# Performance work log

Measured on AMD Instinct MI355X. Metric: run time of the kernel, lower is better.

The kernel has to match this reference:

```python
import jax, jax.numpy as jnp
import numpy as np
import math

EMBED_DIM = 512
NHEAD = 8
HEAD_DIM = EMBED_DIM // NHEAD
B, L = 32, 512
EPS = 1e-5


def layer_norm(x, gamma, beta):
    mu = jnp.mean(x, axis=-1, keepdims=True)
    var = jnp.var(x, axis=-1, keepdims=True)
    return (x - mu) * jax.lax.rsqrt(var + EPS) * gamma + beta


def setup_inputs() -> dict:
    key = jax.random.key(0)
    ks = jax.random.split(key, 16)
    D = EMBED_DIM
    s = 1.0 / math.sqrt(D)
    return {
        "x": jax.random.normal(ks[0], (B, L, D), dtype=jnp.float32),
        "inter": jax.random.normal(ks[1], (B, L, L, 4), dtype=jnp.float32),
        "qkv_w": jax.random.normal(ks[2], (D, 3 * D), dtype=jnp.float32) * s,
        "qkv_b": jnp.zeros((3 * D,), dtype=jnp.float32),
        "out_w": jax.random.normal(ks[3], (D, D), dtype=jnp.float32) * s,
        "out_b": jnp.zeros((D,), dtype=jnp.float32),
        "norm1_g": jnp.ones((D,), dtype=jnp.float32),
        "norm1_b": jnp.zeros((D,), dtype=jnp.float32),
        "norm2_g": jnp.ones((D,), dtype=jnp.float32),
        "norm2_b": jnp.zeros((D,), dtype=jnp.float32),
        "inter_w": jax.random.normal(ks[4], (4, NHEAD), dtype=jnp.float32) * 0.5,
        "ffn_w1": jax.random.normal(ks[5], (D, 4 * D), dtype=jnp.float32) * s,
        "ffn_b1": jnp.zeros((4 * D,), dtype=jnp.float32),
        "ffn_w2": jax.random.normal(ks[6], (4 * D, D), dtype=jnp.float32) * (1.0 / math.sqrt(4 * D)),
        "ffn_b2": jnp.zeros((D,), dtype=jnp.float32),
    }


def reference(x, inter, qkv_w, qkv_b, out_w, out_b, norm1_g, norm1_b,
              norm2_g, norm2_b, inter_w, ffn_w1, ffn_b1, ffn_w2, ffn_b2):
    Bb, Ll, D = x.shape
    residual = x
    h = layer_norm(x, norm1_g, norm1_b)
    qkv = (h @ qkv_w + qkv_b).reshape(Bb, Ll, 3, NHEAD, HEAD_DIM)
    qkv = jnp.transpose(qkv, (2, 0, 3, 1, 4))  # (3, B, H, L, hd)
    q, k, v = qkv[0], qkv[1], qkv[2]
    scale = math.sqrt(HEAD_DIM)
    scores = jnp.einsum("bhqd,bhkd->bhqk", q, k) / scale
    # pairwise interaction bias: (B,L,L,4) @ (4,H) -> (B,H,L,L)
    bias = jnp.einsum("bqkf,fh->bhqk", inter, inter_w)
    attn = jax.nn.softmax(scores + bias, axis=-1)
    # dropout p=0 in eval mode
    out = jnp.einsum("bhqk,bhkd->bhqd", attn, v)
    out = jnp.transpose(out, (0, 2, 1, 3)).reshape(Bb, Ll, D)
    x = residual + out @ out_w + out_b
    h2 = layer_norm(x, norm2_g, norm2_b)
    ffn = jax.nn.gelu(h2 @ ffn_w1 + ffn_b1, approximate=False) @ ffn_w2 + ffn_b2
    return x + ffn
```

## Files before the change

kernel.cpp:

```cpp
#include <hip/hip_runtime.h>
#include <math.h>

#define BB 32
#define LL 512
#define DD 512
#define NH 8
#define HD 64

typedef __attribute__((ext_vector_type(8))) short bf16x8;
typedef __attribute__((ext_vector_type(4))) float f32x4;

__device__ __forceinline__ unsigned short f2bf(float x) {
    union { float f; unsigned u; } v; v.f = x;
    unsigned r = v.u + 0x7fffu + ((v.u >> 16) & 1u);
    return (unsigned short)(r >> 16);
}

__device__ __forceinline__ float warp_sum(float v) {
    #pragma unroll
    for (int o = 32; o > 0; o >>= 1) v += __shfl_down(v, o);
    return v;
}

__global__ void ln_kernel(const float* __restrict__ X, const float* __restrict__ g,
                          const float* __restrict__ b, unsigned short* __restrict__ Y) {
    __shared__ float red[8];
    const size_t base = (size_t)blockIdx.x * DD;
    const int t = threadIdx.x;
    float x0 = X[base + t], x1 = X[base + t + 256];
    float s = warp_sum(x0 + x1);
    float q = warp_sum(x0 * x0 + x1 * x1);
    if ((t & 63) == 0) { red[t >> 6] = s; red[4 + (t >> 6)] = q; }
    __syncthreads();
    float S = red[0] + red[1] + red[2] + red[3];
    float Q = red[4] + red[5] + red[6] + red[7];
    float mu  = S * (1.0f / 512.0f);
    float var = Q * (1.0f / 512.0f) - mu * mu;
    float r = rsqrtf(var + 1e-5f);
    Y[base + t]       = f2bf((x0 - mu) * r * g[t] + b[t]);
    Y[base + t + 256] = f2bf((x1 - mu) * r * g[t + 256] + b[t + 256]);
}

__global__ void transpose_bf16(const float* __restrict__ W, unsigned short* __restrict__ WT,
                               int K, int N) {
    __shared__ float t[32][33];
    const int n0 = blockIdx.x * 32, k0 = blockIdx.y * 32;
    const int tx = threadIdx.x & 31, ty = threadIdx.x >> 5;
    #pragma unroll
    for (int r = 0; r < 32; r += 8)
        t[ty + r][tx] = W[(size_t)(k0 + ty + r) * N + n0 + tx];
    __syncthreads();
    #pragma unroll
    for (int r = 0; r < 32; r += 8)
        WT[(size_t)(n0 + ty + r) * K + k0 + tx] = f2bf(t[tx][ty + r]);
}

template <int ACT, int RES, int OM>
__global__ __launch_bounds__(256)
void gemm_mfma(const unsigned short* __restrict__ A, const unsigned short* __restrict__ BT,
               const float* __restrict__ bias, const float* __restrict__ res,
               void* __restrict__ Cv, unsigned short* __restrict__ kfrag,
               unsigned short* __restrict__ vfrag, int M, int N, int K) {
    __shared__ unsigned short As0[128 * 64];
    __shared__ unsigned short Bs0[128 * 64];
    __shared__ unsigned short As1[128 * 64];
    __shared__ unsigned short Bs1[128 * 64];
    const int tid = threadIdx.x;
    const int wave = tid >> 6, lane = tid & 63;
    const int wm = (wave >> 1) * 64, wn = (wave & 1) * 64;

    const int nx = N >> 7;
    const int chunk = (int)gridDim.x >> 3;
    const int o = ((int)blockIdx.x & 7) * chunk + ((int)blockIdx.x >> 3);
    const int bn = (o % nx) * 128;
    const int bm = (o / nx) * 128;

    f32x4 acc[4][4] = {};

    auto stage = [&](unsigned short* AS, unsigned short* BS, int k0) {
        #pragma unroll
        for (int it = 0; it < 4; ++it) {
            const int s = it * 256 + tid;
            const int row = s >> 3, pch = s & 7;
            const int lch = pch ^ (row & 7);
            const unsigned short* ga = A + (size_t)(bm + row) * K + k0 + lch * 8;
            __builtin_amdgcn_global_load_lds(
                (const __attribute__((address_space(1))) void*)ga,
                (__attribute__((address_space(3))) void*)(AS + s * 8), 16, 0, 0);
            const unsigned short* gb = BT + (size_t)(bn + row) * K + k0 + lch * 8;
            __builtin_amdgcn_global_load_lds(
                (const __attribute__((address_space(1))) void*)gb,
                (__attribute__((address_space(3))) void*)(BS + s * 8), 16, 0, 0);
        }
    };

    auto compute = [&](const unsigned short* AS, const unsigned short* BS) {
        #pragma unroll
        for (int ks = 0; ks < 2; ++ks) {
            bf16x8 af[4], bfr[4];
            #pragma unroll
            for (int i = 0; i < 4; ++i) {
                const int row = wm + i * 16 + (lane & 15);
                const int pch = (ks * 4 + (lane >> 4)) ^ (row & 7);
                af[i] = *(const bf16x8*)(AS + row * 64 + pch * 8);
            }
            #pragma unroll
            for (int j = 0; j < 4; ++j) {
                const int row = wn + j * 16 + (lane & 15);
                const int pch = (ks * 4 + (lane >> 4)) ^ (row & 7);
                bfr[j] = *(const bf16x8*)(BS + row * 64 + pch * 8);
            }
            #pragma unroll
            for (int i = 0; i < 4; ++i)
                #pragma unroll
                for (int j = 0; j < 4; ++j)
                    acc[i][j] = __builtin_amdgcn_mfma_f32_16x16x32_bf16(
                        af[i], bfr[j], acc[i][j], 0, 0, 0);
        }
    };

    stage(As0, Bs0, 0);
    for (int k0 = 0; k0 < K; k0 += 128) {
        __syncthreads();
        if (k0 + 64 < K) stage(As1, Bs1, k0 + 64);
        compute(As0, Bs0);
        __syncthreads();
        if (k0 + 128 < K) stage(As0, Bs0, k0 + 128);
        compute(As1, Bs1);
    }

    const int cl = lane & 15, rq = (lane >> 4) * 4;
    #pragma unroll
    for (int j = 0; j < 4; ++j) {
        const int col = bn + wn + j * 16 + cl;
        const float bv = bias[col];
        #pragma unroll
        for (int i = 0; i < 4; ++i) {
            const int r0 = bm + wm + i * 16 + rq;
            #pragma unroll
            for (int r = 0; r < 4; ++r) {
                float v = acc[i][j][r] + bv;
                if (ACT == 1) v = 0.5f * v * (1.0f + erff(v * 0.70710678118654752f));
                if (RES) v += res[(size_t)(r0 + r) * N + col];
                if (OM == 0) {
                    ((float*)Cv)[(size_t)(r0 + r) * N + col] = v;
                } else if (OM == 1) {
                    ((unsigned short*)Cv)[(size_t)(r0 + r) * N + col] = f2bf(v);
                } else {
                    const int row = r0 + r;
                    const int b = row >> 9, kpos = row & 511;
                    if (col < 512) {
                        ((unsigned short*)Cv)[(size_t)row * 512 + col] = f2bf(v * 0.125f);
                    } else if (col < 1024) {
                        const int h = (col - 512) >> 6, dd = (col - 512) & 63;
                        const int kt = kpos >> 6, jj = (kpos >> 4) & 3, lo2 = kpos & 15;
                        const int kk = dd >> 5, hi2 = (dd >> 3) & 3, e = dd & 7;
                        kfrag[((((size_t)(b * NH + h) * 8 + kt) * 2 + kk) * 4 + jj) * 512
                              + (hi2 * 16 + lo2) * 8 + e] = f2bf(v);
                    } else {
                        const int h = (col - 1024) >> 6, dd = (col - 1024) & 63;
                        const int kt = kpos >> 6, kk = (kpos >> 5) & 1, hi2 = (kpos >> 3) & 3, e = kpos & 7;
                        const int jj = dd >> 4, lo2 = dd & 15;
                        vfrag[((((size_t)(b * NH + h) * 8 + kt) * 2 + kk) * 4 + jj) * 512
                              + (hi2 * 16 + lo2) * 8 + e] = f2bf(v);
                    }
                }
            }
        }
    }
}

__global__ __launch_bounds__(512)
void flash_kernel(const unsigned short* __restrict__ qbuf,
                  const unsigned short* __restrict__ kfrag,
                  const unsigned short* __restrict__ vfrag,
                  const float* __restrict__ inter,
                  const float* __restrict__ iw,
                  unsigned short* __restrict__ O) {
    __shared__ float it[2][16 * 256];
    __shared__ unsigned short plds[8][16 * 72];
    const int qg = blockIdx.x, b = blockIdx.y;
    const int tid = threadIdx.x, wave = tid >> 6, lane = tid & 63;
    const int h = wave;
    const int lo = lane & 15, hi = lane >> 4;

    const float iw0 = iw[h], iw1 = iw[8 + h], iw2 = iw[16 + h], iw3 = iw[24 + h];
    const float* interb = inter + (size_t)b * 512 * 512 * 4;
    unsigned short* pw = &plds[wave][0];

    const unsigned short* qp = qbuf + ((size_t)(b * 512 + qg * 16 + lo)) * 512 + h * 64 + hi * 8;
    const bf16x8 qf0 = *(const bf16x8*)(qp);
    const bf16x8 qf1 = *(const bf16x8*)(qp + 32);

    const unsigned short* kfb = kfrag + (size_t)(b * NH + h) * 32768 + (size_t)lane * 8;
    const unsigned short* vfb = vfrag + (size_t)(b * NH + h) * 32768 + (size_t)lane * 8;

    const int srow0 = wave * 2, srow1 = wave * 2 + 1;
    const float* sg0 = interb + (((size_t)(qg * 16 + srow0)) * 512 + (lane ^ (srow0 & 7))) * 4;
    const float* sg1 = interb + (((size_t)(qg * 16 + srow1)) * 512 + (lane ^ (srow1 & 7))) * 4;

    f32x4 o[4] = {};
    float m = -1e30f, lsum = 0.0f;

    bf16x8 kf[8];
    #pragma unroll
    for (int jj = 0; jj < 8; ++jj)
        kf[jj] = *(const bf16x8*)(kfb + jj * 512);
    __builtin_amdgcn_global_load_lds(
        (const __attribute__((address_space(1))) void*)sg0,
        (__attribute__((address_space(3))) void*)(&it[0][srow0 * 256] + lane * 4), 16, 0, 0);
    __builtin_amdgcn_global_load_lds(
        (const __attribute__((address_space(1))) void*)sg1,
        (__attribute__((address_space(3))) void*)(&it[0][srow1 * 256] + lane * 4), 16, 0, 0);

    #pragma unroll 1
    for (int kt = 0; kt < 8; ++kt) {
        const int buf = kt & 1;
        __syncthreads();
        f32x4 s4[4] = {};
        __builtin_amdgcn_s_setprio(1);
        #pragma unroll
        for (int j = 0; j < 4; ++j)
            s4[j] = __builtin_amdgcn_mfma_f32_16x16x32_bf16(kf[j], qf0, s4[j], 0, 0, 0);
        #pragma unroll
        for (int j = 0; j < 4; ++j)
            s4[j] = __builtin_amdgcn_mfma_f32_16x16x32_bf16(kf[4 + j], qf1, s4[j], 0, 0, 0);
        __builtin_amdgcn_s_setprio(0);
        const unsigned short* vp = vfb + kt * 4096;
        bf16x8 vf[8];
        #pragma unroll
        for (int jj = 0; jj < 8; ++jj)
            vf[jj] = *(const bf16x8*)(vp + jj * 512);
        if (kt < 7) {
            const unsigned short* kp = kfb + (kt + 1) * 4096;
            #pragma unroll
            for (int jj = 0; jj < 8; ++jj)
                kf[jj] = *(const bf16x8*)(kp + jj * 512);
        }
        if (kt < 7) {
            const int kb2 = (kt + 1) * 64;
            __builtin_amdgcn_global_load_lds(
                (const __attribute__((address_space(1))) void*)(sg0 + kb2 * 4),
                (__attribute__((address_space(3))) void*)(&it[buf ^ 1][srow0 * 256] + lane * 4),
                16, 0, 0);
            __builtin_amdgcn_global_load_lds(
                (const __attribute__((address_space(1))) void*)(sg1 + kb2 * 4),
                (__attribute__((address_space(3))) void*)(&it[buf ^ 1][srow1 * 256] + lane * 4),
                16, 0, 0);
        }
        __builtin_amdgcn_sched_barrier(0);
        {
            const float* bb = &it[buf][lo * 256];
            const int x7 = lo & 7;
            #pragma unroll
            for (int j = 0; j < 4; ++j) {
                #pragma unroll
                for (int r = 0; r < 4; ++r) {
                    const int c = (((hi * 4 + r) ^ x7) + j * 16) * 4;
                    const float4 f = *(const float4*)(bb + c);
                    s4[j][r] = s4[j][r] + f.x * iw0 + f.y * iw1 + f.z * iw2 + f.w * iw3;
                }
            }
        }
        float t0 = fmaxf(fmaxf(s4[0][0], s4[0][1]), fmaxf(s4[0][2], s4[0][3]));
        float t1 = fmaxf(fmaxf(s4[1][0], s4[1][1]), fmaxf(s4[1][2], s4[1][3]));
        float t2 = fmaxf(fmaxf(s4[2][0], s4[2][1]), fmaxf(s4[2][2], s4[2][3]));
        float t3 = fmaxf(fmaxf(s4[3][0], s4[3][1]), fmaxf(s4[3][2], s4[3][3]));
        float mx = fmaxf(fmaxf(t0, t1), fmaxf(t2, t3));
        mx = fmaxf(mx, __shfl_xor(mx, 16));
        mx = fmaxf(mx, __shfl_xor(mx, 32));
        const float mn = fmaxf(m, mx);
        const float al = __expf(m - mn);
        m = mn;
        #pragma unroll
        for (int j = 0; j < 4; ++j)
            #pragma unroll
            for (int r = 0; r < 4; ++r)
                s4[j][r] = __expf(s4[j][r] - mn);
        float u0 = (s4[0][0] + s4[0][1]) + (s4[0][2] + s4[0][3]);
        float u1 = (s4[1][0] + s4[1][1]) + (s4[1][2] + s4[1][3]);
        float u2 = (s4[2][0] + s4[2][1]) + (s4[2][2] + s4[2][3]);
        float u3 = (s4[3][0] + s4[3][1]) + (s4[3][2] + s4[3][3]);
        float ts = (u0 + u1) + (u2 + u3);
        ts += __shfl_xor(ts, 16);
        ts += __shfl_xor(ts, 32);
        lsum = lsum * al + ts;
        const float aR0 = __shfl(al, hi * 4 + 0);
        const float aR1 = __shfl(al, hi * 4 + 1);
        const float aR2 = __shfl(al, hi * 4 + 2);
        const float aR3 = __shfl(al, hi * 4 + 3);
        #pragma unroll
        for (int j2 = 0; j2 < 4; ++j2) {
            o[j2][0] *= aR0; o[j2][1] *= aR1; o[j2][2] *= aR2; o[j2][3] *= aR3;
        }
        uint2* pq = (uint2*)(pw + lo * 72);
        #pragma unroll
        for (int j = 0; j < 4; ++j) {
            uint2 d;
            d.x = (unsigned)f2bf(s4[j][0]) | ((unsigned)f2bf(s4[j][1]) << 16);
            d.y = (unsigned)f2bf(s4[j][2]) | ((unsigned)f2bf(s4[j][3]) << 16);
            pq[j * 4 + hi] = d;
        }
        __builtin_amdgcn_s_setprio(1);
        #pragma unroll
        for (int kk = 0; kk < 2; ++kk) {
            const bf16x8 pf = *(const bf16x8*)(pw + lo * 72 + kk * 32 + hi * 8);
            #pragma unroll
            for (int j2 = 0; j2 < 4; ++j2)
                o[j2] = __builtin_amdgcn_mfma_f32_16x16x32_bf16(
                    pf, vf[kk * 4 + j2], o[j2], 0, 0, 0);
        }
        __builtin_amdgcn_s_setprio(0);
    }

    const float iR0 = 1.0f / __shfl(lsum, hi * 4 + 0);
    const float iR1 = 1.0f / __shfl(lsum, hi * 4 + 1);
    const float iR2 = 1.0f / __shfl(lsum, hi * 4 + 2);
    const float iR3 = 1.0f / __shfl(lsum, hi * 4 + 3);
    const int qC0 = qg * 16 + hi * 4;
    #pragma unroll
    for (int j2 = 0; j2 < 4; ++j2) {
        O[(size_t)(b * 512 + qC0 + 0) * 512 + h * 64 + j2 * 16 + lo] = f2bf(o[j2][0] * iR0);
        O[(size_t)(b * 512 + qC0 + 1) * 512 + h * 64 + j2 * 16 + lo] = f2bf(o[j2][1] * iR1);
        O[(size_t)(b * 512 + qC0 + 2) * 512 + h * 64 + j2 * 16 + lo] = f2bf(o[j2][2] * iR2);
        O[(size_t)(b * 512 + qC0 + 3) * 512 + h * 64 + j2 * 16 + lo] = f2bf(o[j2][3] * iR3);
    }
}

extern "C" void kernel_launch(void* const* d_in, const int* in_sizes, int n_in,
                              void* d_out, int out_size, void* d_ws, size_t ws_size,
                              hipStream_t stream) {
    const float* x     = (const float*)d_in[0];
    const float* inter = (const float*)d_in[1];
    const float* qkv_w = (const float*)d_in[2];
    const float* qkv_b = (const float*)d_in[3];
    const float* out_w = (const float*)d_in[4];
    const float* out_b = (const float*)d_in[5];
    const float* n1g   = (const float*)d_in[6];
    const float* n1b   = (const float*)d_in[7];
    const float* n2g   = (const float*)d_in[8];
    const float* n2b   = (const float*)d_in[9];
    const float* iw    = (const float*)d_in[10];
    const float* fw1   = (const float*)d_in[11];
    const float* fb1   = (const float*)d_in[12];
    const float* fw2   = (const float*)d_in[13];
    const float* fb2   = (const float*)d_in[14];
    float* out = (float*)d_out;

    if (ws_size < 190840832ull) return;
    char* ws = (char*)d_ws;
    unsigned short* qbuf    = (unsigned short*)(ws);
    unsigned short* kfrag   = (unsigned short*)(ws + 16777216ull);
    unsigned short* vfrag   = (unsigned short*)(ws + 33554432ull);
    unsigned short* attnout = (unsigned short*)(ws + 50331648ull);
    float*          x2      = (float*)(ws + 67108864ull);
    unsigned short* h_bf    = (unsigned short*)(ws + 100663296ull);
    unsigned short* ffnmid  = (unsigned short*)(ws + 117440512ull);
    unsigned short* qkv_wT  = (unsigned short*)(ws + 184549376ull);
    unsigned short* out_wT  = (unsigned short*)(ws + 186122240ull);
    unsigned short* fw1T    = (unsigned short*)(ws + 186646528ull);
    unsigned short* fw2T    = (unsigned short*)(ws + 188743680ull);

    const int M = BB * LL;

    transpose_bf16<<<dim3(1536 / 32, 512 / 32), 256, 0, stream>>>(qkv_w, qkv_wT, 512, 1536);
    transpose_bf16<<<dim3(512 / 32, 512 / 32), 256, 0, stream>>>(out_w, out_wT, 512, 512);
    transpose_bf16<<<dim3(2048 / 32, 512 / 32), 256, 0, stream>>>(fw1, fw1T, 512, 2048);
    transpose_bf16<<<dim3(512 / 32, 2048 / 32), 256, 0, stream>>>(fw2, fw2T, 2048, 512);
    ln_kernel<<<M, 256, 0, stream>>>(x, n1g, n1b, h_bf);
    gemm_mfma<0, 0, 2><<<dim3((1536 / 128) * (M / 128)), 256, 0, stream>>>(
        h_bf, qkv_wT, qkv_b, nullptr, qbuf, kfrag, vfrag, M, 1536, 512);
    flash_kernel<<<dim3(LL / 16, BB), 512, 0, stream>>>(qbuf, kfrag, vfrag, inter, iw, attnout);
    gemm_mfma<0, 1, 0><<<dim3((512 / 128) * (M / 128)), 256, 0, stream>>>(
        attnout, out_wT, out_b, x, x2, nullptr, nullptr, M, 512, 512);
    ln_kernel<<<M, 256, 0, stream>>>(x2, n2g, n2b, h_bf);
    gemm_mfma<1, 0, 1><<<dim3((2048 / 128) * (M / 128)), 256, 0, stream>>>(
        h_bf, fw1T, fb1, nullptr, ffnmid, nullptr, nullptr, M, 2048, 512);
    gemm_mfma<0, 1, 0><<<dim3((512 / 128) * (M / 128)), 256, 0, stream>>>(
        ffnmid, fw2T, fb2, x2, out, nullptr, nullptr, M, 512, 2048);
}
```

Measured before the change: 543.7 us.

## Merge weight transposes into one launch, add lazy softmax rescale, reorder K loads

Replaces the four weight-transpose launches with a single kernel that picks its matrix from the block index, which cuts launch overhead. In the flash kernel, the online-softmax rescale of the output and sum now runs only when the running max grows by more than a threshold. This saves exp and shuffle work on most tiles, at some risk of larger intermediate values. K fragments are now loaded per iteration instead of being prefetched one tile ahead, which removes the prefetch and may expose load latency. The GEMM epilogue is moved into a helper function without changing its behaviour.

```diff
diff --git a/kernel.cpp b/kernel.cpp
--- a/kernel.cpp
+++ b/kernel.cpp
@@ -41,10 +41,19 @@
     Y[base + t + 256] = f2bf((x1 - mu) * r * g[t + 256] + b[t + 256]);
 }
 
-__global__ void transpose_bf16(const float* __restrict__ W, unsigned short* __restrict__ WT,
-                               int K, int N) {
+__global__ void transpose_all(const float* __restrict__ qkv_w, unsigned short* __restrict__ qkv_wT,
+                              const float* __restrict__ out_w, unsigned short* __restrict__ out_wT,
+                              const float* __restrict__ fw1,   unsigned short* __restrict__ fw1T,
+                              const float* __restrict__ fw2,   unsigned short* __restrict__ fw2T) {
     __shared__ float t[32][33];
-    const int n0 = blockIdx.x * 32, k0 = blockIdx.y * 32;
+    int bid = blockIdx.x;
+    const float* W; unsigned short* WT; int K, N, tile;
+    if (bid < 768)       { W = qkv_w; WT = qkv_wT; K = 512;  N = 1536; tile = bid; }
+    else if (bid < 1024) { W = out_w; WT = out_wT; K = 512;  N = 512;  tile = bid - 768; }
+    else if (bid < 2048) { W = fw1;   WT = fw1T;   K = 512;  N = 2048; tile = bid - 1024; }
+    else                 { W = fw2;   WT = fw2T;   K = 2048; N = 512;  tile = bid - 2048; }
+    const int nx = N >> 5;
+    const int n0 = (tile % nx) * 32, k0 = (tile / nx) * 32;
     const int tx = threadIdx.x & 31, ty = threadIdx.x >> 5;
     #pragma unroll
     for (int r = 0; r < 32; r += 8)
@@ -53,6 +62,37 @@
     #pragma unroll
     for (int r = 0; r < 32; r += 8)
         WT[(size_t)(n0 + ty + r) * K + k0 + tx] = f2bf(t[tx][ty + r]);
+}
+
+template <int ACT, int RES, int OM>
+__device__ __forceinline__ void epi_store(
+    float v, int row, int col, int N,
+    const float* __restrict__ res, void* __restrict__ Cv,
+    unsigned short* __restrict__ kfrag, unsigned short* __restrict__ vfrag) {
+    if (ACT == 1) v = 0.5f * v * (1.0f + erff(v * 0.70710678118654752f));
+    if (RES) v += res[(size_t)row * N + col];
+    if (OM == 0) {
+        ((float*)Cv)[(size_t)row * N + col] = v;
+    } else if (OM == 1) {
+        ((unsigned short*)Cv)[(size_t)row * N + col] = f2bf(v);
+    } else {
+        const int b = row >> 9, kpos = row & 511;
+        if (col < 512) {
+            ((unsigned short*)Cv)[(size_t)row * 512 + col] = f2bf(v * 0.125f);
+        } else if (col < 1024) {
+            const int h = (col - 512) >> 6, dd = (col - 512) & 63;
+            const int kt = kpos >> 6, jj = (kpos >> 4) & 3, lo2 = kpos & 15;
+            const int kk = dd >> 5, hi2 = (dd >> 3) & 3, e = dd & 7;
+            kfrag[((((size_t)(b * NH + h) * 8 + kt) * 2 + kk) * 4 + jj) * 512
+                  + (hi2 * 16 + lo2) * 8 + e] = f2bf(v);
+        } else {
+            const int h = (col - 1024) >> 6, dd = (col - 1024) & 63;
+            const int kt = kpos >> 6, kk = (kpos >> 5) & 1, hi2 = (kpos >> 3) & 3, e = kpos & 7;
+            const int jj = dd >> 4, lo2 = dd & 15;
+            vfrag[((((size_t)(b * NH + h) * 8 + kt) * 2 + kk) * 4 + jj) * 512
+                  + (hi2 * 16 + lo2) * 8 + e] = f2bf(v);
+        }
+    }
 }
 
 template <int ACT, int RES, int OM>
@@ -138,34 +178,8 @@
         for (int i = 0; i < 4; ++i) {
             const int r0 = bm + wm + i * 16 + rq;
             #pragma unroll
-            for (int r = 0; r < 4; ++r) {
-                float v = acc[i][j][r] + bv;
-                if (ACT == 1) v = 0.5f * v * (1.0f + erff(v * 0.70710678118654752f));
-                if (RES) v += res[(size_t)(r0 + r) * N + col];
-                if (OM == 0) {
-                    ((float*)Cv)[(size_t)(r0 + r) * N + col] = v;
-                } else if (OM == 1) {
-                    ((unsigned short*)Cv)[(size_t)(r0 + r) * N + col] = f2bf(v);
-                } else {
-                    const int row = r0 + r;
-                    const int b = row >> 9, kpos = row & 511;
-                    if (col < 512) {
-                        ((unsigned short*)Cv)[(size_t)row * 512 + col] = f2bf(v * 0.125f);
-                    } else if (col < 1024) {
-                        const int h = (col - 512) >> 6, dd = (col - 512) & 63;
-                        const int kt = kpos >> 6, jj = (kpos >> 4) & 3, lo2 = kpos & 15;
-                        const int kk = dd >> 5, hi2 = (dd >> 3) & 3, e = dd & 7;
-                        kfrag[((((size_t)(b * NH + h) * 8 + kt) * 2 + kk) * 4 + jj) * 512
-                              + (hi2 * 16 + lo2) * 8 + e] = f2bf(v);
-                    } else {
-                        const int h = (col - 1024) >> 6, dd = (col - 1024) & 63;
-                        const int kt = kpos >> 6, kk = (kpos >> 5) & 1, hi2 = (kpos >> 3) & 3, e = kpos & 7;
-                        const int jj = dd >> 4, lo2 = dd & 15;
-                        vfrag[((((size_t)(b * NH + h) * 8 + kt) * 2 + kk) * 4 + jj) * 512
-                              + (hi2 * 16 + lo2) * 8 + e] = f2bf(v);
-                    }
-                }
-            }
+            for (int r = 0; r < 4; ++r)
+                epi_store<ACT, RES, OM>(acc[i][j][r] + bv, r0 + r, col, N, res, Cv, kfrag, vfrag);
         }
     }
 }
@@ -202,10 +216,6 @@
     f32x4 o[4] = {};
     float m = -1e30f, lsum = 0.0f;
 
-    bf16x8 kf[8];
-    #pragma unroll
-    for (int jj = 0; jj < 8; ++jj)
-        kf[jj] = *(const bf16x8*)(kfb + jj * 512);
     __builtin_amdgcn_global_load_lds(
         (const __attribute__((address_space(1))) void*)sg0,
         (__attribute__((address_space(3))) void*)(&it[0][srow0 * 256] + lane * 4), 16, 0, 0);
@@ -217,26 +227,16 @@
     for (int kt = 0; kt < 8; ++kt) {
         const int buf = kt & 1;
         __syncthreads();
-        f32x4 s4[4] = {};
-        __builtin_amdgcn_s_setprio(1);
-        #pragma unroll
-        for (int j = 0; j < 4; ++j)
-            s4[j] = __builtin_amdgcn_mfma_f32_16x16x32_bf16(kf[j], qf0, s4[j], 0, 0, 0);
-        #pragma unroll
-        for (int j = 0; j < 4; ++j)
-            s4[j] = __builtin_amdgcn_mfma_f32_16x16x32_bf16(kf[4 + j], qf1, s4[j], 0, 0, 0);
-        __builtin_amdgcn_s_setprio(0);
+        const unsigned short* kp = kfb + kt * 4096;
+        bf16x8 kf[8];
+        #pragma unroll
+        for (int jj = 0; jj < 8; ++jj)
+            kf[jj] = *(const bf16x8*)(kp + jj * 512);
         const unsigned short* vp = vfb + kt * 4096;
         bf16x8 vf[8];
         #pragma unroll
         for (int jj = 0; jj < 8; ++jj)
             vf[jj] = *(const bf16x8*)(vp + jj * 512);
-        if (kt < 7) {
-            const unsigned short* kp = kfb + (kt + 1) * 4096;
-            #pragma unroll
-            for (int jj = 0; jj < 8; ++jj)
-                kf[jj] = *(const bf16x8*)(kp + jj * 512);
-        }
         if (kt < 7) {
             const int kb2 = (kt + 1) * 64;
             __builtin_amdgcn_global_load_lds(
@@ -249,6 +249,15 @@
                 16, 0, 0);
         }
         __builtin_amdgcn_sched_barrier(0);
+        f32x4 s4[4] = {};
+        __builtin_amdgcn_s_setprio(1);
+        #pragma unroll
+        for (int j = 0; j < 4; ++j)
+            s4[j] = __builtin_amdgcn_mfma_f32_16x16x32_bf16(kf[j], qf0, s4[j], 0, 0, 0);
+        #pragma unroll
+        for (int j = 0; j < 4; ++j)
+            s4[j] = __builtin_amdgcn_mfma_f32_16x16x32_bf16(kf[4 + j], qf1, s4[j], 0, 0, 0);
+        __builtin_amdgcn_s_setprio(0);
         {
             const float* bb = &it[buf][lo * 256];
             const int x7 = lo & 7;
@@ -269,14 +278,25 @@
         float mx = fmaxf(fmaxf(t0, t1), fmaxf(t2, t3));
         mx = fmaxf(mx, __shfl_xor(mx, 16));
         mx = fmaxf(mx, __shfl_xor(mx, 32));
-        const float mn = fmaxf(m, mx);
-        const float al = __expf(m - mn);
-        m = mn;
+        if (!__all((mx - m) <= 8.0f)) {
+            const float mn = fmaxf(m, mx);
+            const float al = __expf(m - mn);
+            m = mn;
+            lsum *= al;
+            const float aR0 = __shfl(al, hi * 4 + 0);
+            const float aR1 = __shfl(al, hi * 4 + 1);
+            const float aR2 = __shfl(al, hi * 4 + 2);
+            const float aR3 = __shfl(al, hi * 4 + 3);
+            #pragma unroll
+            for (int j2 = 0; j2 < 4; ++j2) {
+                o[j2][0] *= aR0; o[j2][1] *= aR1; o[j2][2] *= aR2; o[j2][3] *= aR3;
+            }
+        }
         #pragma unroll
         for (int j = 0; j < 4; ++j)
             #pragma unroll
             for (int r = 0; r < 4; ++r)
-                s4[j][r] = __expf(s4[j][r] - mn);
+                s4[j][r] = __expf(s4[j][r] - m);
         float u0 = (s4[0][0] + s4[0][1]) + (s4[0][2] + s4[0][3]);
         float u1 = (s4[1][0] + s4[1][1]) + (s4[1][2] + s4[1][3]);
         float u2 = (s4[2][0] + s4[2][1]) + (s4[2][2] + s4[2][3]);
@@ -284,15 +304,7 @@
         float ts = (u0 + u1) + (u2 + u3);
         ts += __shfl_xor(ts, 16);
         ts += __shfl_xor(ts, 32);
-        lsum = lsum * al + ts;
-        const float aR0 = __shfl(al, hi * 4 + 0);
-        const float aR1 = __shfl(al, hi * 4 + 1);
-        const float aR2 = __shfl(al, hi * 4 + 2);
-        const float aR3 = __shfl(al, hi * 4 + 3);
-        #pragma unroll
-        for (int j2 = 0; j2 < 4; ++j2) {
-            o[j2][0] *= aR0; o[j2][1] *= aR1; o[j2][2] *= aR2; o[j2][3] *= aR3;
-        }
+        lsum += ts;
         uint2* pq = (uint2*)(pw + lo * 72);
         #pragma unroll
         for (int j = 0; j < 4; ++j) {
@@ -363,10 +375,8 @@
 
     const int M = BB * LL;
 
-    transpose_bf16<<<dim3(1536 / 32, 512 / 32), 256, 0, stream>>>(qkv_w, qkv_wT, 512, 1536);
-    transpose_bf16<<<dim3(512 / 32, 512 / 32), 256, 0, stream>>>(out_w, out_wT, 512, 512);
-    transpose_bf16<<<dim3(2048 / 32, 512 / 32), 256, 0, stream>>>(fw1, fw1T, 512, 2048);
-    transpose_bf16<<<dim3(512 / 32, 2048 / 32), 256, 0, stream>>>(fw2, fw2T, 2048, 512);
+    transpose_all<<<dim3(3072), 256, 0, stream>>>(qkv_w, qkv_wT, out_w, out_wT,
+                                                  fw1, fw1T, fw2, fw2T);
     ln_kernel<<<M, 256, 0, stream>>>(x, n1g, n1b, h_bf);
     gemm_mfma<0, 0, 2><<<dim3((1536 / 128) * (M / 128)), 256, 0, stream>>>(
         h_bf, qkv_wT, qkv_b, nullptr, qbuf, kfrag, vfrag, M, 1536, 512);
```

After: 499.4 us. 1.09x faster.
